# Performance work log

Measured on AMD Instinct MI355X. Metric: run time of the kernel, lower is better.

Reference implementation:

```python
import jax, jax.numpy as jnp
import numpy as np

WINDOW = 127          # odd
W = (WINDOW - 1) // 2 # 63 half-window
Q_CH = WINDOW + 1     # 128 query chunk
K_CH = WINDOW * 2     # 254 key chunk


def _compl_mod(m, n):
    return int(n * int(np.ceil(m / n)) - m)


def setup_inputs() -> dict:
    key = jax.random.key(0)
    kq, kk, kv = jax.random.split(key, 3)
    B, L, NH, H = 4, 4096, 16, 64
    return {
        "q": jax.random.normal(kq, (B, L, NH, H), dtype=jnp.float32),
        "k": jax.random.normal(kk, (B, L, NH, H), dtype=jnp.float32),
        "v": jax.random.normal(kv, (B, L, NH, H), dtype=jnp.float32),
    }


def _build_mask(c, k_pad, dtype_bool=bool):
    # base band mask over one (q_ch, k_ch) block: True = masked out
    u = jnp.triu(jnp.ones((Q_CH, K_CH), dtype=bool))
    band = jnp.logical_and(u, jnp.flip(u, (0, 1)))
    base = ~band
    mask_left = base.at[:, :W].set(True)
    mask_right = base.at[:, K_CH - (W + k_pad):].set(True)
    if c > 1:
        mid = jnp.broadcast_to(base, (c - 2, Q_CH, K_CH)) if c > 2 else jnp.zeros((0, Q_CH, K_CH), bool)
        return jnp.concatenate([mask_left[None], mid, mask_right[None]], axis=0)
    return jnp.logical_or(mask_left, mask_right)[None]


def reference(q, k, v):
    b, s, nh, h = q.shape
    q = q * (h ** -0.5)

    q_pad = _compl_mod(s, Q_CH)
    k_pad = _compl_mod(s + 2 * W - K_CH, Q_CH)

    # chunk queries: (b, c, q_ch, nh, h)
    qp = jnp.pad(q, ((0, 0), (0, q_pad), (0, 0), (0, 0)))
    c = (s + q_pad) // Q_CH
    qw = qp.reshape(b, c, Q_CH, nh, h)

    # overlapping key/value windows via gather: (b, c, k_ch, nh, h)
    kp = jnp.pad(k, ((0, 0), (W, W + k_pad), (0, 0), (0, 0)))
    vp = jnp.pad(v, ((0, 0), (W, W + k_pad), (0, 0), (0, 0)))
    starts = np.arange(c) * Q_CH
    idx = starts[:, None] + np.arange(K_CH)[None, :]  # (c, k_ch)
    kw = kp[:, idx]
    vw = vp[:, idx]

    # block scores: (b, nh, c, q_ch, k_ch)
    A = jnp.einsum('bcqnh,bcknh->bncqk', qw, kw)

    mask = _build_mask(c, k_pad)  # (c, q_ch, k_ch)
    neg = -jnp.finfo(A.dtype).max
    A = jnp.where(mask[None, None], neg, A)
    A = jax.nn.softmax(A, axis=-1)

    z = jnp.einsum('bncqk,bcknh->bncqh', A, vw)  # (b, nh, c, q_ch, h)
    z = z.reshape(b, nh, c * Q_CH, h)[:, :, :s]
    return jnp.transpose(z, (0, 2, 1, 3))  # (b, s, nh, h)
```

## Files before the change

kernel.cpp:

```cpp
#include <hip/hip_runtime.h>


typedef _Float16 f16;
typedef _Float16 f16x2  __attribute__((ext_vector_type(2)));
typedef _Float16 f16x4  __attribute__((ext_vector_type(4)));
typedef _Float16 f16x8  __attribute__((ext_vector_type(8)));
typedef float    f32x16 __attribute__((ext_vector_type(16)));
typedef int      int4v  __attribute__((ext_vector_type(4)));

constexpr int NB = 4, L = 4096, NH = 16, H = 64;
constexpr int CQ = 256, NC = L / CQ, KW = 384, WR = 63;
constexpr int RS = NH * H;

constexpr int K_OFF = 0;
constexpr int V_OFF = 32768;
constexpr int LDS_BYTES = 65536;

#define DEV static __device__ __forceinline__

DEV int iclamp(int x, int lo, int hi) { return x < lo ? lo : (x > hi ? hi : x); }

DEV float fexp2(float x) {
#if __has_builtin(__builtin_amdgcn_exp2f)
    return __builtin_amdgcn_exp2f(x);
#else
    return exp2f(x);
#endif
}

DEV int packh2(float a, float b) {
    f16x2 p; p.x = (f16)a; p.y = (f16)b;
    return __builtin_bit_cast(int, p);
}

DEV int kaddr(int rr, int colb) {
    return K_OFF + rr * 128 + (colb ^ ((rr & 7) << 4));
}

DEV int vaddr(int h, int kb) {
    return V_OFF + ((h * 512 + kb) ^ ((((h & 7) ^ ((h >> 3) & 7))) << 4));
}

DEV void swap_halves(int& a, int& b) {
    asm volatile("v_permlane32_swap_b32 %0, %1" : "+v"(a), "+v"(b));
}

__global__ __launch_bounds__(512, 4)
void wattn_kernel(const float* __restrict__ q_, const float* __restrict__ k_,
                  const float* __restrict__ v_, float* __restrict__ o_)
{
    __shared__ alignas(16) char smem[LDS_BYTES];

    const int bid = (int)blockIdx.x;
    const int wid = (bid & 7) * ((NB * NH * NC) / 8) + (bid >> 3);
    const int c = wid & (NC - 1);
    const int n = (wid >> 4) & (NH - 1);
    const int b = wid >> 8;

    const int t    = (int)threadIdx.x;
    const int lane = t & 63;
    const int w    = t >> 6;
    const int lq   = lane & 31;
    const int hi   = lane >> 5;

    const int kg0 = c * CQ - WR;
    const size_t bn = ((size_t)b * L * NH + n) * H;
    const float qs = 0.125f * 1.44269504088896f;

    const int h4 = (t & 15) << 2;
    const int cb = h4 << 1;
    const int ru = t >> 4;

    const int iq = w * 32 + lq;
    const float* qrow = q_ + bn + (size_t)(c * CQ + iq) * RS + hi * 8;
    f16x8 qf[4];
    #pragma unroll
    for (int tq = 0; tq < 4; ++tq) {
        float4 a  = *(const float4*)(qrow + tq * 16);
        float4 b2 = *(const float4*)(qrow + tq * 16 + 4);
        qf[tq] = (f16x8){(f16)(a.x * qs),  (f16)(a.y * qs),  (f16)(a.z * qs),  (f16)(a.w * qs),
                         (f16)(b2.x * qs), (f16)(b2.y * qs), (f16)(b2.z * qs), (f16)(b2.w * qs)};
    }

    #pragma unroll
    for (int p = 0; p < 8; ++p) {
        int r  = ru + p * 32;
        int kr = iclamp(kg0 + r, 0, L - 1);
        float4 x = *(const float4*)(k_ + bn + (size_t)kr * RS + h4);
        *(f16x4*)(smem + kaddr(r, cb)) = (f16x4){(f16)x.x, (f16)x.y, (f16)x.z, (f16)x.w};
    }
    #pragma unroll
    for (int p = 0; p < 4; ++p) {
        int r0  = ru * 2 + p * 64;
        int kr0 = iclamp(kg0 + r0,     0, L - 1);
        int kr1 = iclamp(kg0 + r0 + 1, 0, L - 1);
        float4 v0 = *(const float4*)(v_ + bn + (size_t)kr0 * RS + h4);
        float4 v1 = *(const float4*)(v_ + bn + (size_t)kr1 * RS + h4);
        int kb = r0 * 2;
        *(f16x2*)(smem + vaddr(h4 + 0, kb)) = (f16x2){(f16)v0.x, (f16)v1.x};
        *(f16x2*)(smem + vaddr(h4 + 1, kb)) = (f16x2){(f16)v0.y, (f16)v1.y};
        *(f16x2*)(smem + vaddr(h4 + 2, kb)) = (f16x2){(f16)v0.z, (f16)v1.z};
        *(f16x2*)(smem + vaddr(h4 + 3, kb)) = (f16x2){(f16)v0.w, (f16)v1.w};
    }

    const int jlo = (c == 0) ? WR : 0;
    const int jhi = (KW < L - kg0) ? KW : (L - kg0);
    const int lo  = (iq > jlo) ? iq : jlo;
    const int hb  = (iq + 126 < jhi - 1) ? (iq + 126) : (jhi - 1);
    const unsigned span = (unsigned)(hb - lo);

    f32x16 o0, o1;
    #pragma unroll
    for (int r = 0; r < 16; ++r) { o0[r] = 0.f; o1[r] = 0.f; }
    float dsum = 0.f;

    auto body = [&](int kt) {
        const int rr = (kt & 7) * 32 + lq;
        f16x8 kf[4];
        #pragma unroll
        for (int tq = 0; tq < 4; ++tq)
            kf[tq] = *(const f16x8*)(smem + kaddr(rr, 32 * tq + 16 * hi));

        f32x16 s;
        #pragma unroll
        for (int r = 0; r < 16; ++r) s[r] = 0.f;
        #pragma unroll
        for (int tq = 0; tq < 4; ++tq)
            s = __builtin_amdgcn_mfma_f32_32x32x16_f16(kf[tq], qf[tq], s, 0, 0, 0);

        const int jb = kt * 32 + 4 * hi;
        float pe[16];
        #pragma unroll
        for (int r = 0; r < 16; ++r) {
            int j = jb + (r & 3) + ((r >> 2) << 3);
            float e = fexp2(s[r]);
            e = ((unsigned)(j - lo) <= span) ? e : 0.f;
            dsum += e;
            pe[r] = e;
        }
        int d0 = packh2(pe[0],  pe[1]),  d1 = packh2(pe[2],  pe[3]);
        int d2 = packh2(pe[4],  pe[5]),  d3 = packh2(pe[6],  pe[7]);
        int d4 = packh2(pe[8],  pe[9]),  d5 = packh2(pe[10], pe[11]);
        int d6 = packh2(pe[12], pe[13]), d7 = packh2(pe[14], pe[15]);
        swap_halves(d0, d2); swap_halves(d1, d3);
        swap_halves(d4, d6); swap_halves(d5, d7);
        f16x8 pa0 = __builtin_bit_cast(f16x8, (int4v){d0, d1, d2, d3});
        f16x8 pa1 = __builtin_bit_cast(f16x8, (int4v){d4, d5, d6, d7});

        const int kb = (kt & 7) * 64 + hi * 16;
        f16x8 vb00 = *(const f16x8*)(smem + vaddr(lq,      kb));
        f16x8 vb01 = *(const f16x8*)(smem + vaddr(lq,      kb + 32));
        f16x8 vb10 = *(const f16x8*)(smem + vaddr(32 + lq, kb));
        f16x8 vb11 = *(const f16x8*)(smem + vaddr(32 + lq, kb + 32));
        o0 = __builtin_amdgcn_mfma_f32_32x32x16_f16(vb00, pa0, o0, 0, 0, 0);
        o0 = __builtin_amdgcn_mfma_f32_32x32x16_f16(vb01, pa1, o0, 0, 0, 0);
        o1 = __builtin_amdgcn_mfma_f32_32x32x16_f16(vb10, pa0, o1, 0, 0, 0);
        o1 = __builtin_amdgcn_mfma_f32_32x32x16_f16(vb11, pa1, o1, 0, 0, 0);
    };

    auto epilogue = [&]() {
        float dtot = dsum + __shfl_xor(dsum, 32, 64);
        float dinv = 1.0f / dtot;
        const size_t ob = ((size_t)b * L + (size_t)c * CQ) * RS + (size_t)n * H;
        float* orow = o_ + ob + (size_t)iq * RS;
        #pragma unroll
        for (int m = 0; m < 4; ++m) {
            int h0 = 8 * m + 4 * hi;
            float4 v0, v1;
            v0.x = o0[4 * m + 0] * dinv;  v0.y = o0[4 * m + 1] * dinv;
            v0.z = o0[4 * m + 2] * dinv;  v0.w = o0[4 * m + 3] * dinv;
            v1.x = o1[4 * m + 0] * dinv;  v1.y = o1[4 * m + 1] * dinv;
            v1.z = o1[4 * m + 2] * dinv;  v1.w = o1[4 * m + 3] * dinv;
            *(float4*)(orow + h0)      = v0;
            *(float4*)(orow + 32 + h0) = v1;
        }
    };

    __syncthreads();

    {
        const int kend = (w + 4 < 7) ? (w + 4) : 7;
        for (int kt = w; kt <= kend; ++kt) body(kt);
    }
    if (w < 4) epilogue();

    __syncthreads();

    #pragma unroll
    for (int p = 0; p < 4; ++p) {
        int r  = 256 + ru + p * 32;
        int kr = iclamp(kg0 + r, 0, L - 1);
        float4 x = *(const float4*)(k_ + bn + (size_t)kr * RS + h4);
        *(f16x4*)(smem + kaddr(r - 256, cb)) = (f16x4){(f16)x.x, (f16)x.y, (f16)x.z, (f16)x.w};
    }
    #pragma unroll
    for (int p = 0; p < 2; ++p) {
        int r0  = 256 + ru * 2 + p * 64;
        int kr0 = iclamp(kg0 + r0,     0, L - 1);
        int kr1 = iclamp(kg0 + r0 + 1, 0, L - 1);
        float4 v0 = *(const float4*)(v_ + bn + (size_t)kr0 * RS + h4);
        float4 v1 = *(const float4*)(v_ + bn + (size_t)kr1 * RS + h4);
        int kb = (r0 - 256) * 2;
        *(f16x2*)(smem + vaddr(h4 + 0, kb)) = (f16x2){(f16)v0.x, (f16)v1.x};
        *(f16x2*)(smem + vaddr(h4 + 1, kb)) = (f16x2){(f16)v0.y, (f16)v1.y};
        *(f16x2*)(smem + vaddr(h4 + 2, kb)) = (f16x2){(f16)v0.z, (f16)v1.z};
        *(f16x2*)(smem + vaddr(h4 + 3, kb)) = (f16x2){(f16)v0.w, (f16)v1.w};
    }

    __syncthreads();

    if (w >= 4) {
        for (int kt = 8; kt <= w + 4; ++kt) body(kt);
        epilogue();
    }
}

extern "C" void kernel_launch(void* const* d_in, const int* in_sizes, int n_in,
                              void* d_out, int out_size, void* d_ws, size_t ws_size,
                              hipStream_t stream) {
    const float* q = (const float*)d_in[0];
    const float* k = (const float*)d_in[1];
    const float* v = (const float*)d_in[2];
    float* o = (float*)d_out;
    (void)in_sizes; (void)n_in; (void)out_size; (void)d_ws; (void)ws_size;
    wattn_kernel<<<dim3(NB * NH * NC), dim3(512), 0, stream>>>(q, k, v, o);
}
```

Before: 55.02 us.

## Process four 128-query chunks per block with a rolling K/V tile ring

Each block of 256 threads now walks four consecutive 128-query chunks and keeps an 8-slot ring of 32-row K/V tiles in LDS. After the first chunk only four new tiles are staged, so overlapping window rows are reused instead of reloaded. This cuts redundant global reads and fp16 conversion work compared with the single 256-query chunk per block. The cost is fewer, serial blocks (512 instead of 1024) with a barrier per chunk and no overlap between loading and compute, which may lower latency hiding.

```diff
diff --git a/kernel.cpp b/kernel.cpp
--- a/kernel.cpp
+++ b/kernel.cpp
@@ -9,7 +9,10 @@
 typedef int      int4v  __attribute__((ext_vector_type(4)));
 
 constexpr int NB = 4, L = 4096, NH = 16, H = 64;
-constexpr int CQ = 256, NC = L / CQ, KW = 384, WR = 63;
+constexpr int CQ = 128, NC = L / CQ, KW = 256, WR = 63;
+constexpr int CPB = 4;
+constexpr int NCG = NC / CPB;
+constexpr int NBLK = NB * NH * NCG;
 constexpr int RS = NH * H;
 
 constexpr int K_OFF = 0;
@@ -45,17 +48,18 @@
     asm volatile("v_permlane32_swap_b32 %0, %1" : "+v"(a), "+v"(b));
 }
 
-__global__ __launch_bounds__(512, 4)
+__global__ __launch_bounds__(256, 2)
 void wattn_kernel(const float* __restrict__ q_, const float* __restrict__ k_,
                   const float* __restrict__ v_, float* __restrict__ o_)
 {
     __shared__ alignas(16) char smem[LDS_BYTES];
 
     const int bid = (int)blockIdx.x;
-    const int wid = (bid & 7) * ((NB * NH * NC) / 8) + (bid >> 3);
-    const int c = wid & (NC - 1);
-    const int n = (wid >> 4) & (NH - 1);
-    const int b = wid >> 8;
+    const int wid = (bid & 7) * (NBLK / 8) + (bid >> 3);
+    const int cg = wid & (NCG - 1);
+    const int n  = (wid >> 3) & (NH - 1);
+    const int b  = wid >> 7;
+    const int c0 = cg * CPB;
 
     const int t    = (int)threadIdx.x;
     const int lane = t & 63;
@@ -63,155 +67,135 @@
     const int lq   = lane & 31;
     const int hi   = lane >> 5;
 
-    const int kg0 = c * CQ - WR;
     const size_t bn = ((size_t)b * L * NH + n) * H;
     const float qs = 0.125f * 1.44269504088896f;
+    const int base = c0 * CQ - WR;
 
     const int h4 = (t & 15) << 2;
     const int cb = h4 << 1;
     const int ru = t >> 4;
 
-    const int iq = w * 32 + lq;
-    const float* qrow = q_ + bn + (size_t)(c * CQ + iq) * RS + hi * 8;
-    f16x8 qf[4];
-    #pragma unroll
-    for (int tq = 0; tq < 4; ++tq) {
-        float4 a  = *(const float4*)(qrow + tq * 16);
-        float4 b2 = *(const float4*)(qrow + tq * 16 + 4);
-        qf[tq] = (f16x8){(f16)(a.x * qs),  (f16)(a.y * qs),  (f16)(a.z * qs),  (f16)(a.w * qs),
-                         (f16)(b2.x * qs), (f16)(b2.y * qs), (f16)(b2.z * qs), (f16)(b2.w * qs)};
-    }
-
-    #pragma unroll
-    for (int p = 0; p < 8; ++p) {
-        int r  = ru + p * 32;
-        int kr = iclamp(kg0 + r, 0, L - 1);
-        float4 x = *(const float4*)(k_ + bn + (size_t)kr * RS + h4);
-        *(f16x4*)(smem + kaddr(r, cb)) = (f16x4){(f16)x.x, (f16)x.y, (f16)x.z, (f16)x.w};
-    }
-    #pragma unroll
-    for (int p = 0; p < 4; ++p) {
-        int r0  = ru * 2 + p * 64;
-        int kr0 = iclamp(kg0 + r0,     0, L - 1);
-        int kr1 = iclamp(kg0 + r0 + 1, 0, L - 1);
-        float4 v0 = *(const float4*)(v_ + bn + (size_t)kr0 * RS + h4);
-        float4 v1 = *(const float4*)(v_ + bn + (size_t)kr1 * RS + h4);
-        int kb = r0 * 2;
-        *(f16x2*)(smem + vaddr(h4 + 0, kb)) = (f16x2){(f16)v0.x, (f16)v1.x};
-        *(f16x2*)(smem + vaddr(h4 + 1, kb)) = (f16x2){(f16)v0.y, (f16)v1.y};
-        *(f16x2*)(smem + vaddr(h4 + 2, kb)) = (f16x2){(f16)v0.z, (f16)v1.z};
-        *(f16x2*)(smem + vaddr(h4 + 3, kb)) = (f16x2){(f16)v0.w, (f16)v1.w};
-    }
-
-    const int jlo = (c == 0) ? WR : 0;
-    const int jhi = (KW < L - kg0) ? KW : (L - kg0);
-    const int lo  = (iq > jlo) ? iq : jlo;
-    const int hb  = (iq + 126 < jhi - 1) ? (iq + 126) : (jhi - 1);
-    const unsigned span = (unsigned)(hb - lo);
-
-    f32x16 o0, o1;
-    #pragma unroll
-    for (int r = 0; r < 16; ++r) { o0[r] = 0.f; o1[r] = 0.f; }
-    float dsum = 0.f;
-
-    auto body = [&](int kt) {
-        const int rr = (kt & 7) * 32 + lq;
-        f16x8 kf[4];
+    auto stage_tile = [&](int G) {
+        const int slot = G & 7;
         #pragma unroll
-        for (int tq = 0; tq < 4; ++tq)
-            kf[tq] = *(const f16x8*)(smem + kaddr(rr, 32 * tq + 16 * hi));
-
-        f32x16 s;
+        for (int p = 0; p < 2; ++p) {
+            int r  = ru + p * 16;
+            int kr = iclamp(base + G * 32 + r, 0, L - 1);
+            float4 x = *(const float4*)(k_ + bn + (size_t)kr * RS + h4);
+            *(f16x4*)(smem + kaddr(slot * 32 + r, cb)) =
+                (f16x4){(f16)x.x, (f16)x.y, (f16)x.z, (f16)x.w};
+        }
+        {
+            int r0  = ru * 2;
+            int kr0 = iclamp(base + G * 32 + r0,     0, L - 1);
+            int kr1 = iclamp(base + G * 32 + r0 + 1, 0, L - 1);
+            float4 v0 = *(const float4*)(v_ + bn + (size_t)kr0 * RS + h4);
+            float4 v1 = *(const float4*)(v_ + bn + (size_t)kr1 * RS + h4);
+            int kb = slot * 64 + r0 * 2;
+            *(f16x2*)(smem + vaddr(h4 + 0, kb)) = (f16x2){(f16)v0.x, (f16)v1.x};
+            *(f16x2*)(smem + vaddr(h4 + 1, kb)) = (f16x2){(f16)v0.y, (f16)v1.y};
+            *(f16x2*)(smem + vaddr(h4 + 2, kb)) = (f16x2){(f16)v0.z, (f16)v1.z};
+            *(f16x2*)(smem + vaddr(h4 + 3, kb)) = (f16x2){(f16)v0.w, (f16)v1.w};
+        }
+    };
+
+    #pragma unroll 1
+    for (int ci = 0; ci < CPB; ++ci) {
+        const int c = c0 + ci;
+
+        const int gA = (ci == 0) ? 0 : 4 * ci + 4;
+        const int gB = 4 * ci + 7;
+        for (int G = gA; G <= gB; ++G) stage_tile(G);
+
+        const int iq = w * 32 + lq;
+        const float* qrow = q_ + bn + (size_t)(c * CQ + iq) * RS + hi * 8;
+        f16x8 qf[4];
         #pragma unroll
-        for (int r = 0; r < 16; ++r) s[r] = 0.f;
+        for (int tq = 0; tq < 4; ++tq) {
+            float4 a  = *(const float4*)(qrow + tq * 16);
+            float4 b2 = *(const float4*)(qrow + tq * 16 + 4);
+            qf[tq] = (f16x8){(f16)(a.x * qs),  (f16)(a.y * qs),  (f16)(a.z * qs),  (f16)(a.w * qs),
+                             (f16)(b2.x * qs), (f16)(b2.y * qs), (f16)(b2.z * qs), (f16)(b2.w * qs)};
+        }
+
+        const int kg0 = c * CQ - WR;
+        const int jlo = (c == 0) ? WR : 0;
+        const int jhi = (KW < L - kg0) ? KW : (L - kg0);
+        const int lo  = (iq > jlo) ? iq : jlo;
+        const int hb  = (iq + 126 < jhi - 1) ? (iq + 126) : (jhi - 1);
+        const unsigned span = (unsigned)(hb - lo);
+
+        f32x16 o0, o1;
         #pragma unroll
-        for (int tq = 0; tq < 4; ++tq)
-            s = __builtin_amdgcn_mfma_f32_32x32x16_f16(kf[tq], qf[tq], s, 0, 0, 0);
-
-        const int jb = kt * 32 + 4 * hi;
-        float pe[16];
-        #pragma unroll
-        for (int r = 0; r < 16; ++r) {
-            int j = jb + (r & 3) + ((r >> 2) << 3);
-            float e = fexp2(s[r]);
-            e = ((unsigned)(j - lo) <= span) ? e : 0.f;
-            dsum += e;
-            pe[r] = e;
-        }
-        int d0 = packh2(pe[0],  pe[1]),  d1 = packh2(pe[2],  pe[3]);
-        int d2 = packh2(pe[4],  pe[5]),  d3 = packh2(pe[6],  pe[7]);
-        int d4 = packh2(pe[8],  pe[9]),  d5 = packh2(pe[10], pe[11]);
-        int d6 = packh2(pe[12], pe[13]), d7 = packh2(pe[14], pe[15]);
-        swap_halves(d0, d2); swap_halves(d1, d3);
-        swap_halves(d4, d6); swap_halves(d5, d7);
-        f16x8 pa0 = __builtin_bit_cast(f16x8, (int4v){d0, d1, d2, d3});
-        f16x8 pa1 = __builtin_bit_cast(f16x8, (int4v){d4, d5, d6, d7});
-
-        const int kb = (kt & 7) * 64 + hi * 16;
-        f16x8 vb00 = *(const f16x8*)(smem + vaddr(lq,      kb));
-        f16x8 vb01 = *(const f16x8*)(smem + vaddr(lq,      kb + 32));
-        f16x8 vb10 = *(const f16x8*)(smem + vaddr(32 + lq, kb));
-        f16x8 vb11 = *(const f16x8*)(smem + vaddr(32 + lq, kb + 32));
-        o0 = __builtin_amdgcn_mfma_f32_32x32x16_f16(vb00, pa0, o0, 0, 0, 0);
-        o0 = __builtin_amdgcn_mfma_f32_32x32x16_f16(vb01, pa1, o0, 0, 0, 0);
-        o1 = __builtin_amdgcn_mfma_f32_32x32x16_f16(vb10, pa0, o1, 0, 0, 0);
-        o1 = __builtin_amdgcn_mfma_f32_32x32x16_f16(vb11, pa1, o1, 0, 0, 0);
-    };
-
-    auto epilogue = [&]() {
-        float dtot = dsum + __shfl_xor(dsum, 32, 64);
-        float dinv = 1.0f / dtot;
-        const size_t ob = ((size_t)b * L + (size_t)c * CQ) * RS + (size_t)n * H;
-        float* orow = o_ + ob + (size_t)iq * RS;
-        #pragma unroll
-        for (int m = 0; m < 4; ++m) {
-            int h0 = 8 * m + 4 * hi;
-            float4 v0, v1;
-            v0.x = o0[4 * m + 0] * dinv;  v0.y = o0[4 * m + 1] * dinv;
-            v0.z = o0[4 * m + 2] * dinv;  v0.w = o0[4 * m + 3] * dinv;
-            v1.x = o1[4 * m + 0] * dinv;  v1.y = o1[4 * m + 1] * dinv;
-            v1.z = o1[4 * m + 2] * dinv;  v1.w = o1[4 * m + 3] * dinv;
-            *(float4*)(orow + h0)      = v0;
-            *(float4*)(orow + 32 + h0) = v1;
-        }
-    };
-
-    __syncthreads();
-
-    {
-        const int kend = (w + 4 < 7) ? (w + 4) : 7;
-        for (int kt = w; kt <= kend; ++kt) body(kt);
-    }
-    if (w < 4) epilogue();
-
-    __syncthreads();
-
-    #pragma unroll
-    for (int p = 0; p < 4; ++p) {
-        int r  = 256 + ru + p * 32;
-        int kr = iclamp(kg0 + r, 0, L - 1);
-        float4 x = *(const float4*)(k_ + bn + (size_t)kr * RS + h4);
-        *(f16x4*)(smem + kaddr(r - 256, cb)) = (f16x4){(f16)x.x, (f16)x.y, (f16)x.z, (f16)x.w};
-    }
-    #pragma unroll
-    for (int p = 0; p < 2; ++p) {
-        int r0  = 256 + ru * 2 + p * 64;
-        int kr0 = iclamp(kg0 + r0,     0, L - 1);
-        int kr1 = iclamp(kg0 + r0 + 1, 0, L - 1);
-        float4 v0 = *(const float4*)(v_ + bn + (size_t)kr0 * RS + h4);
-        float4 v1 = *(const float4*)(v_ + bn + (size_t)kr1 * RS + h4);
-        int kb = (r0 - 256) * 2;
-        *(f16x2*)(smem + vaddr(h4 + 0, kb)) = (f16x2){(f16)v0.x, (f16)v1.x};
-        *(f16x2*)(smem + vaddr(h4 + 1, kb)) = (f16x2){(f16)v0.y, (f16)v1.y};
-        *(f16x2*)(smem + vaddr(h4 + 2, kb)) = (f16x2){(f16)v0.z, (f16)v1.z};
-        *(f16x2*)(smem + vaddr(h4 + 3, kb)) = (f16x2){(f16)v0.w, (f16)v1.w};
-    }
-
-    __syncthreads();
-
-    if (w >= 4) {
-        for (int kt = 8; kt <= w + 4; ++kt) body(kt);
-        epilogue();
+        for (int r = 0; r < 16; ++r) { o0[r] = 0.f; o1[r] = 0.f; }
+        float dsum = 0.f;
+
+        __syncthreads();
+
+        for (int tl = w; tl <= w + 4; ++tl) {
+            const int slot = (4 * ci + tl) & 7;
+            const int rr   = slot * 32 + lq;
+            f16x8 kf[4];
+            #pragma unroll
+            for (int tq = 0; tq < 4; ++tq)
+                kf[tq] = *(const f16x8*)(smem + kaddr(rr, 32 * tq + 16 * hi));
+
+            f32x16 s;
+            #pragma unroll
+            for (int r = 0; r < 16; ++r) s[r] = 0.f;
+            #pragma unroll
+            for (int tq = 0; tq < 4; ++tq)
+                s = __builtin_amdgcn_mfma_f32_32x32x16_f16(kf[tq], qf[tq], s, 0, 0, 0);
+
+            const int jb = tl * 32 + 4 * hi;
+            float pe[16];
+            #pragma unroll
+            for (int r = 0; r < 16; ++r) {
+                int j = jb + (r & 3) + ((r >> 2) << 3);
+                float e = fexp2(s[r]);
+                e = ((unsigned)(j - lo) <= span) ? e : 0.f;
+                dsum += e;
+                pe[r] = e;
+            }
+            int d0 = packh2(pe[0],  pe[1]),  d1 = packh2(pe[2],  pe[3]);
+            int d2 = packh2(pe[4],  pe[5]),  d3 = packh2(pe[6],  pe[7]);
+            int d4 = packh2(pe[8],  pe[9]),  d5 = packh2(pe[10], pe[11]);
+            int d6 = packh2(pe[12], pe[13]), d7 = packh2(pe[14], pe[15]);
+            swap_halves(d0, d2); swap_halves(d1, d3);
+            swap_halves(d4, d6); swap_halves(d5, d7);
+            f16x8 pa0 = __builtin_bit_cast(f16x8, (int4v){d0, d1, d2, d3});
+            f16x8 pa1 = __builtin_bit_cast(f16x8, (int4v){d4, d5, d6, d7});
+
+            const int kb = slot * 64 + hi * 16;
+            f16x8 vb00 = *(const f16x8*)(smem + vaddr(lq,      kb));
+            f16x8 vb01 = *(const f16x8*)(smem + vaddr(lq,      kb + 32));
+            f16x8 vb10 = *(const f16x8*)(smem + vaddr(32 + lq, kb));
+            f16x8 vb11 = *(const f16x8*)(smem + vaddr(32 + lq, kb + 32));
+            o0 = __builtin_amdgcn_mfma_f32_32x32x16_f16(vb00, pa0, o0, 0, 0, 0);
+            o0 = __builtin_amdgcn_mfma_f32_32x32x16_f16(vb01, pa1, o0, 0, 0, 0);
+            o1 = __builtin_amdgcn_mfma_f32_32x32x16_f16(vb10, pa0, o1, 0, 0, 0);
+            o1 = __builtin_amdgcn_mfma_f32_32x32x16_f16(vb11, pa1, o1, 0, 0, 0);
+        }
+
+        {
+            float dtot = dsum + __shfl_xor(dsum, 32, 64);
+            float dinv = 1.0f / dtot;
+            const size_t ob = ((size_t)b * L + (size_t)c * CQ) * RS + (size_t)n * H;
+            float* orow = o_ + ob + (size_t)iq * RS;
+            #pragma unroll
+            for (int m = 0; m < 4; ++m) {
+                int h0 = 8 * m + 4 * hi;
+                float4 v0, v1;
+                v0.x = o0[4 * m + 0] * dinv;  v0.y = o0[4 * m + 1] * dinv;
+                v0.z = o0[4 * m + 2] * dinv;  v0.w = o0[4 * m + 3] * dinv;
+                v1.x = o1[4 * m + 0] * dinv;  v1.y = o1[4 * m + 1] * dinv;
+                v1.z = o1[4 * m + 2] * dinv;  v1.w = o1[4 * m + 3] * dinv;
+                *(float4*)(orow + h0)      = v0;
+                *(float4*)(orow + 32 + h0) = v1;
+            }
+        }
+
+        __syncthreads();
     }
 }
 
@@ -223,5 +207,5 @@
     const float* v = (const float*)d_in[2];
     float* o = (float*)d_out;
     (void)in_sizes; (void)n_in; (void)out_size; (void)d_ws; (void)ws_size;
-    wattn_kernel<<<dim3(NB * NH * NC), dim3(512), 0, stream>>>(q, k, v, o);
-}
+    wattn_kernel<<<dim3(NBLK), dim3(256), 0, stream>>>(q, k, v, o);
+}
```

Measured after the change: 52.04 us. 5.4% less time.
